# Kernel tuning notes

Measured on AMD Instinct MI355X. Metric: run time of the kernel, lower is better.

## Reference

```python
import jax, jax.numpy as jnp
import numpy as np

B, T, D, H, NL, V = 2, 2048, 512, 8, 4, 32000
HD = D // H
EPS = 1e-5


def _ln(x, g, b):
    mu = jnp.mean(x, axis=-1, keepdims=True)
    var = jnp.var(x, axis=-1, keepdims=True)
    return (x - mu) * jax.lax.rsqrt(var + EPS) * g + b


def setup_inputs() -> dict:
    key = jax.random.key(0)
    ks = jax.random.split(key, 16)
    f = lambda k, shp: jax.random.normal(k, shp, jnp.float32) * 0.02
    return {
        "token_ids": jax.random.randint(ks[0], (B, T), 0, V),
        "labels": jax.random.randint(ks[1], (B, T), 0, V),
        "tok_emb": f(ks[2], (V, D)),
        "pos_emb": f(ks[3], (T, D)),
        "Wq": f(ks[4], (NL, H, D, HD)),
        "Wk": f(ks[5], (NL, H, D, HD)),
        "Wv": f(ks[6], (NL, H, D, HD)),
        "Wo": f(ks[7], (NL, D, D)),
        "bo": jnp.zeros((NL, D), jnp.float32),
        "ln1_g": jnp.ones((NL, D), jnp.float32),
        "ln1_b": jnp.zeros((NL, D), jnp.float32),
        "ln2_g": jnp.ones((NL, D), jnp.float32),
        "ln2_b": jnp.zeros((NL, D), jnp.float32),
        "W1": f(ks[8], (NL, D, 4 * D)),
        "b1": jnp.zeros((NL, 4 * D), jnp.float32),
        "W2": f(ks[9], (NL, 4 * D, D)),
        "b2": jnp.zeros((NL, D), jnp.float32),
        "lnf_g": jnp.ones((D,), jnp.float32),
        "lnf_b": jnp.zeros((D,), jnp.float32),
        "Wp": f(ks[10], (D, V)),
        "bp": jnp.zeros((V,), jnp.float32),
    }


def reference(token_ids, labels, tok_emb, pos_emb, Wq, Wk, Wv, Wo, bo,
              ln1_g, ln1_b, ln2_g, ln2_b, W1, b1, W2, b2, lnf_g, lnf_b, Wp, bp):
    x = tok_emb[token_ids] + pos_emb[:T]            # (B, T, D)
    causal = jnp.tril(jnp.ones((T, T), bool))       # tril buffer
    scale = D ** -0.5                               # NOTE: source scales by dim_embed, not head_size
    for l in range(NL):
        xn = _ln(x, ln1_g[l], ln1_b[l])
        q = jnp.einsum('btd,hde->bhte', xn, Wq[l])  # (B, H, T, HD)
        k = jnp.einsum('btd,hde->bhte', xn, Wk[l])
        v = jnp.einsum('btd,hde->bhte', xn, Wv[l])
        w = jnp.einsum('bhte,bhse->bhts', q, k) * scale
        w = jnp.where(causal, w, -jnp.inf)
        w = jax.nn.softmax(w, axis=-1)
        o = jnp.einsum('bhts,bhse->bhte', w, v)     # (B, H, T, HD)
        o = o.transpose(0, 2, 1, 3).reshape(B, T, D)  # concat heads
        x = x + o @ Wo[l] + bo[l]
        xn = _ln(x, ln2_g[l], ln2_b[l])
        x = x + jax.nn.relu(xn @ W1[l] + b1[l]) @ W2[l] + b2[l]
    x = _ln(x, lnf_g, lnf_b)
    logits = x @ Wp + bp                            # (B, T, V)
    logits2d = logits.reshape(B * T, V)
    logp = jax.nn.log_softmax(logits2d, axis=-1)
    loss = -jnp.mean(logp[jnp.arange(B * T), labels.reshape(B * T)])
    return logits2d, loss
```

## Files before the change

### kernel.cpp

```cpp
#include <hip/hip_runtime.h>
#include <hip/hip_bf16.h>
#include <math.h>

#define B_ 2
#define T_ 2048
#define D_ 512
#define H_ 8
#define NL_ 4
#define V_ 32000
#define HD_ 64
#define BT_ (B_*T_)
#define EPS_ 1e-5f
#define SCALE_ 0.04419417382415922f
#define NEGBIG -1e30f

typedef __bf16 bf16x8 __attribute__((ext_vector_type(8)));
typedef float  f32x4  __attribute__((ext_vector_type(4)));

__device__ __forceinline__ unsigned short f2bf(float f) {
  union { float f; unsigned u; } v; v.f = f;
  unsigned r = v.u + 0x7fff + ((v.u >> 16) & 1);
  return (unsigned short)(r >> 16);
}
__device__ __forceinline__ float bf2f(unsigned short h) {
  union { unsigned u; float f; } c; c.u = ((unsigned)h) << 16; return c.f;
}

__device__ __forceinline__ void gl_lds16(const void* g, void* l) {
  __builtin_amdgcn_global_load_lds(
      (const __attribute__((address_space(1))) void*)g,
      (__attribute__((address_space(3))) void*)l, 16, 0, 0);
}

#define WAITVM(n) asm volatile("s_waitcnt vmcnt(" #n ")" ::: "memory")
#define WAITLG0   asm volatile("s_waitcnt lgkmcnt(0)" ::: "memory")

__global__ __launch_bounds__(256) void embed_kernel(
    const int* __restrict__ ids, const float* __restrict__ tok,
    const float* __restrict__ pos, unsigned short* __restrict__ x)
{
  int i = blockIdx.x * 256 + threadIdx.x;
  int c8 = i & 63;
  int bt = i >> 6;
  int t  = bt & (T_ - 1);
  const float4* tr = reinterpret_cast<const float4*>(tok + (size_t)ids[bt] * D_ + c8*8);
  const float4* pr = reinterpret_cast<const float4*>(pos + (size_t)t * D_ + c8*8);
  float4 a0 = tr[0], a1 = tr[1], p0 = pr[0], p1 = pr[1];
  ushort4 o0, o1;
  o0.x = f2bf(a0.x + p0.x); o0.y = f2bf(a0.y + p0.y);
  o0.z = f2bf(a0.z + p0.z); o0.w = f2bf(a0.w + p0.w);
  o1.x = f2bf(a1.x + p1.x); o1.y = f2bf(a1.y + p1.y);
  o1.z = f2bf(a1.z + p1.z); o1.w = f2bf(a1.w + p1.w);
  unsigned short* orow = x + (size_t)bt * D_ + c8*8;
  *reinterpret_cast<ushort4*>(orow)     = o0;
  *reinterpret_cast<ushort4*>(orow + 4) = o1;
}

__global__ __launch_bounds__(256) void ln_kernel(
    const unsigned short* __restrict__ x, const float* __restrict__ g,
    const float* __restrict__ b, unsigned short* __restrict__ out)
{
  int row  = blockIdx.x * 4 + (threadIdx.x >> 6);
  int lane = threadIdx.x & 63;
  const unsigned short* xr = x + (size_t)row * D_;
  ushort4 u0 = *reinterpret_cast<const ushort4*>(xr + lane*4);
  ushort4 u1 = *reinterpret_cast<const ushort4*>(xr + 256 + lane*4);
  float v0x = bf2f(u0.x), v0y = bf2f(u0.y), v0z = bf2f(u0.z), v0w = bf2f(u0.w);
  float v1x = bf2f(u1.x), v1y = bf2f(u1.y), v1z = bf2f(u1.z), v1w = bf2f(u1.w);
  float s = v0x + v0y + v0z + v0w + v1x + v1y + v1z + v1w;
  float q = v0x*v0x + v0y*v0y + v0z*v0z + v0w*v0w
          + v1x*v1x + v1y*v1y + v1z*v1z + v1w*v1w;
  #pragma unroll
  for (int off = 1; off < 64; off <<= 1) {
    s += __shfl_xor(s, off);
    q += __shfl_xor(q, off);
  }
  float mean = s * (1.0f / D_);
  float var  = q * (1.0f / D_) - mean * mean;
  float rs   = rsqrtf(var + EPS_);
  const float4* g4 = reinterpret_cast<const float4*>(g);
  const float4* b4 = reinterpret_cast<const float4*>(b);
  float4 gv0 = g4[lane], gv1 = g4[lane + 64];
  float4 bv0 = b4[lane], bv1 = b4[lane + 64];
  ushort4 p0, p1;
  p0.x = f2bf((v0x - mean) * rs * gv0.x + bv0.x);
  p0.y = f2bf((v0y - mean) * rs * gv0.y + bv0.y);
  p0.z = f2bf((v0z - mean) * rs * gv0.z + bv0.z);
  p0.w = f2bf((v0w - mean) * rs * gv0.w + bv0.w);
  p1.x = f2bf((v1x - mean) * rs * gv1.x + bv1.x);
  p1.y = f2bf((v1y - mean) * rs * gv1.y + bv1.y);
  p1.z = f2bf((v1z - mean) * rs * gv1.z + bv1.z);
  p1.w = f2bf((v1w - mean) * rs * gv1.w + bv1.w);
  unsigned short* orow = out + (size_t)row * D_;
  *reinterpret_cast<ushort4*>(orow + lane * 4)       = p0;
  *reinterpret_cast<ushort4*>(orow + 256 + lane * 4) = p1;
}

__global__ __launch_bounds__(256) void transpose_cast(
    const float* __restrict__ src, unsigned short* __restrict__ dst,
    int C, int R, long sstride, long dstride)
{
  src += (size_t)blockIdx.z * sstride;
  dst += (size_t)blockIdx.z * dstride;
  __shared__ float t[32][33];
  int r0 = blockIdx.x * 32, c0 = blockIdx.y * 32;
  int tx = threadIdx.x & 31, ty = threadIdx.x >> 5;
  #pragma unroll
  for (int i = 0; i < 4; i++)
    t[ty + i*8][tx] = src[(size_t)(r0 + ty + i*8) * C + c0 + tx];
  __syncthreads();
  #pragma unroll
  for (int i = 0; i < 4; i++)
    dst[(size_t)(c0 + ty + i*8) * R + r0 + tx] = f2bf(t[tx][ty + i*8]);
}

__global__ __launch_bounds__(256) void qkvw_transpose(
    const float* __restrict__ Wq, const float* __restrict__ Wk,
    const float* __restrict__ Wv, unsigned short* __restrict__ dst)
{
  int z = blockIdx.z; int l = z / 24; int rem = z % 24; int mat = rem >> 3; int h = rem & 7;
  const float* W = (mat == 0 ? Wq : (mat == 1 ? Wk : Wv)) + ((size_t)(l * 8 + h)) * D_ * HD_;
  unsigned short* d = dst + ((size_t)l * 1536 + mat * 512 + h * 64) * D_;
  __shared__ float t[32][33];
  int d0 = blockIdx.x * 32, e0 = blockIdx.y * 32;
  int tx = threadIdx.x & 31, ty = threadIdx.x >> 5;
  #pragma unroll
  for (int i = 0; i < 4; i++)
    t[ty + i*8][tx] = W[(size_t)(d0 + ty + i*8) * HD_ + e0 + tx];
  __syncthreads();
  #pragma unroll
  for (int i = 0; i < 4; i++)
    d[(size_t)(e0 + ty + i*8) * D_ + d0 + tx] = f2bf(t[tx][ty + i*8]);
}

__global__ __launch_bounds__(512, 4) void gemm_logits(
    const unsigned short* __restrict__ A,
    const unsigned short* __restrict__ Bt,
    int K, const float* __restrict__ bias,
    float* __restrict__ outF, int ldc,
    float2* __restrict__ ms, int npan)
{
  __shared__ __align__(16) char smem[49152];
  unsigned short* Abase = (unsigned short*)smem;
  unsigned short* Bbase = (unsigned short*)(smem + 16384);
  float* E = (float*)smem;
  float2* msL = (float2*)smem;

  const int tid = threadIdx.x;
  const int lane = tid & 63;
  const int lr = lane & 15, g = lane >> 4;
  const int wv = tid >> 6, wm = wv >> 2, wn = wv & 3;

  const int gx = gridDim.x;
  int id = blockIdx.y * gx + blockIdx.x;
  const int nwg = gx * gridDim.y;
  if ((nwg & 7) == 0) { const int q = nwg >> 3; id = (id & 7) * q + (id >> 3); }
  const int bm = (id % gx) * 128, bn = (id / gx) * 256, bnp = id / gx;

  const int schk = (lane & 3) ^ ((lane >> 3) & 3);
  const unsigned short* Ab = A  + (size_t)(bm + wv*16 + (lane >> 2)) * K + schk * 8;
  const unsigned short* Bb = Bt + (size_t)(bn + wv*16 + (lane >> 2)) * K + schk * 8;

#define STAGEL(s, sl)                                                       \
  { const int kof_ = (s) * 32;                                              \
    gl_lds16(Ab + kof_,                 Abase + (sl)*4096 + wv*512);        \
    gl_lds16(Bb + kof_,                 Bbase + (sl)*8192 + wv*512);        \
    gl_lds16(Bb + (size_t)128*K + kof_, Bbase + (sl)*8192 + 4096 + wv*512); }

  f32x4 acc[4][4];
  #pragma unroll
  for (int m = 0; m < 4; m++)
    #pragma unroll
    for (int n = 0; n < 4; n++)
      acc[m][n] = (f32x4){0.f, 0.f, 0.f, 0.f};

  const int nt = K >> 5;
  STAGEL(0, 0);

  const int slotx = (g ^ ((lr >> 1) & 3)) << 3;

  for (int t = 0; t < nt; ++t) {
    __builtin_amdgcn_sched_barrier(0);
    if (t + 1 < nt) { STAGEL(t + 1, (t + 1) & 1); WAITVM(3); }
    else            { WAITVM(0); }
    __builtin_amdgcn_sched_barrier(0);
    __builtin_amdgcn_s_barrier();
    __builtin_amdgcn_sched_barrier(0);

    const unsigned short* Ac = Abase + (t & 1)*4096;
    const unsigned short* Bc = Bbase + (t & 1)*8192;
    bf16x8 af[4], bfr[4];
    #pragma unroll
    for (int m = 0; m < 4; m++)
      af[m] = *reinterpret_cast<const bf16x8*>(&Ac[(wm*64 + m*16 + lr) * 32 + slotx]);
    #pragma unroll
    for (int n = 0; n < 4; n++)
      bfr[n] = *reinterpret_cast<const bf16x8*>(&Bc[(wn*64 + n*16 + lr) * 32 + slotx]);
    __builtin_amdgcn_s_setprio(1);
    #pragma unroll
    for (int m = 0; m < 4; m++)
      #pragma unroll
      for (int n = 0; n < 4; n++)
        acc[m][n] = __builtin_amdgcn_mfma_f32_16x16x32_bf16(af[m], bfr[n], acc[m][n], 0, 0, 0);
    __builtin_amdgcn_s_setprio(0);
    __builtin_amdgcn_sched_barrier(0);
    __builtin_amdgcn_s_barrier();
  }
#undef STAGEL

  #pragma unroll
  for (int n = 0; n < 4; n++) {
    const float bv = bias ? bias[bn + wn*64 + n*16 + lr] : 0.f;
    #pragma unroll
    for (int m = 0; m < 4; m++)
      #pragma unroll
      for (int r = 0; r < 4; r++)
        acc[m][n][r] += bv;
  }

  if (ms) {
    #pragma unroll
    for (int m = 0; m < 4; m++) {
      float vmax[4] = {NEGBIG, NEGBIG, NEGBIG, NEGBIG};
      #pragma unroll
      for (int n = 0; n < 4; n++)
        #pragma unroll
        for (int r = 0; r < 4; r++)
          vmax[r] = fmaxf(vmax[r], acc[m][n][r]);
      #pragma unroll
      for (int r = 0; r < 4; r++) {
        #pragma unroll
        for (int off = 1; off < 16; off <<= 1)
          vmax[r] = fmaxf(vmax[r], __shfl_xor(vmax[r], off));
      }
      float vsum[4] = {0.f, 0.f, 0.f, 0.f};
      #pragma unroll
      for (int n = 0; n < 4; n++)
        #pragma unroll
        for (int r = 0; r < 4; r++)
          vsum[r] += __expf(acc[m][n][r] - vmax[r]);
      #pragma unroll
      for (int r = 0; r < 4; r++) {
        #pragma unroll
        for (int off = 1; off < 16; off <<= 1)
          vsum[r] += __shfl_xor(vsum[r], off);
      }
      if (lr == 0) {
        #pragma unroll
        for (int r = 0; r < 4; r++)
          msL[(wm*64 + m*16 + g*4 + r) * 4 + wn] = make_float2(vmax[r], vsum[r]);
      }
    }
    __syncthreads();
    if (tid < 128) {
      float M = NEGBIG, S = 0.f;
      #pragma unroll
      for (int w = 0; w < 4; w++) {
        float2 e = msL[tid * 4 + w];
        float Mn = fmaxf(M, e.x);
        S = S * __expf(M - Mn) + e.y * __expf(e.x - Mn);
        M = Mn;
      }
      ms[(size_t)(bm + tid) * npan + bnp] = make_float2(M, S);
    }
  }

  #pragma unroll
  for (int c = 0; c < 4; ++c) {
    __syncthreads();
    if (wm == (c >> 1)) {
      const int mb = (c & 1) * 2;
      #pragma unroll
      for (int mm = 0; mm < 2; mm++)
        #pragma unroll
        for (int n = 0; n < 4; n++)
          #pragma unroll
          for (int r = 0; r < 4; r++)
            E[(mm*16 + g*4 + r) * 260 + wn*64 + n*16 + lr] = acc[mb + mm][n][r];
    }
    __syncthreads();
    #pragma unroll
    for (int rep = 0; rep < 4; rep++) {
      const int row = rep*8 + wv;
      f32x4 v = *reinterpret_cast<const f32x4*>(&E[row*260 + lane*4]);
      __builtin_nontemporal_store(
          v, reinterpret_cast<f32x4*>(&outF[(size_t)(bm + c*32 + row) * ldc + bn + lane*4]));
    }
  }
}

template<int BM_T, int BN_T, int WM, int WN>
__global__ __launch_bounds__(256) void gemm_pipe(
    const unsigned short* __restrict__ A,
    const unsigned short* __restrict__ Bt,
    int K,
    const float* __restrict__ bias,
    const unsigned short* __restrict__ resid,
    float* __restrict__ outF,
    unsigned short* __restrict__ outH,
    int ldc, int relu)
{
  constexpr int BKp = 64;
  constexpr int ALOADS = BM_T / 32;
  constexpr int BLOADS = BN_T / 32;
  constexpr int LOADS  = ALOADS + BLOADS;
  constexpr int MR = BM_T / (16 * WM);
  constexpr int NR = BN_T / (16 * WN);
  __shared__ __align__(16) unsigned short As[2][BM_T * BKp];
  __shared__ __align__(16) unsigned short Bs[2][BN_T * BKp];

  const int tid = threadIdx.x;
  const int lane = tid & 63, wv = tid >> 6;
  const int lr = lane & 15, g = lane >> 4;

  const int gx = gridDim.x;
  int id = blockIdx.y * gx + blockIdx.x;
  const int nwg = gx * gridDim.y;
  if ((nwg & 7) == 0) {
    const int q = nwg >> 3;
    id = (id & 7) * q + (id >> 3);
  }
  const int bm = (id % gx) * BM_T, bn = (id / gx) * BN_T;

  const int m0w = (wv / WN) * (BM_T / WM);
  const int n0w = (wv % WN) * (BN_T / WN);

  const int srow = wv*8 + (lane >> 3);
  const int schk = (lane & 7) ^ (lane >> 3);
  const unsigned short* Ab = A  + (size_t)(bm + srow) * K + schk * 8;
  const unsigned short* Bb = Bt + (size_t)(bn + srow) * K + schk * 8;

#define STAGEP(s, sl)                                                           \
  { const int kof_ = (s) * BKp;                                                 \
    _Pragma("unroll")                                                           \
    for (int i_ = 0; i_ < ALOADS; ++i_)                                         \
      gl_lds16(Ab + (size_t)(i_*32)*K + kof_, As[sl] + i_*2048 + wv*512);       \
    _Pragma("unroll")                                                           \
    for (int i_ = 0; i_ < BLOADS; ++i_)                                         \
      gl_lds16(Bb + (size_t)(i_*32)*K + kof_, Bs[sl] + i_*2048 + wv*512); }

  f32x4 acc[MR][NR];
  #pragma unroll
  for (int m = 0; m < MR; m++)
    #pragma unroll
    for (int n = 0; n < NR; n++)
      acc[m][n] = (f32x4){0.f, 0.f, 0.f, 0.f};

  const int nt = K >> 6;
  STAGEP(0, 0);

  for (int t = 0; t < nt; ++t) {
    __builtin_amdgcn_sched_barrier(0);
    if (t + 1 < nt) {
      STAGEP(t + 1, (t + 1) & 1);
      if constexpr (LOADS == 4) WAITVM(4);
      else if constexpr (LOADS == 6) WAITVM(6);
      else WAITVM(8);
    } else {
      WAITVM(0);
    }
    __builtin_amdgcn_sched_barrier(0);
    __builtin_amdgcn_s_barrier();
    __builtin_amdgcn_sched_barrier(0);

    const unsigned short* Ac = As[t & 1];
    const unsigned short* Bc = Bs[t & 1];
    #pragma unroll
    for (int kk = 0; kk < 2; ++kk) {
      const int sl = ((kk*4 + g) ^ (lr & 7)) << 3;
      bf16x8 af[MR], bfr[NR];
      #pragma unroll
      for (int m = 0; m < MR; m++)
        af[m] = *reinterpret_cast<const bf16x8*>(&Ac[(m0w + m*16 + lr) * BKp + sl]);
      #pragma unroll
      for (int n = 0; n < NR; n++)
        bfr[n] = *reinterpret_cast<const bf16x8*>(&Bc[(n0w + n*16 + lr) * BKp + sl]);
      __builtin_amdgcn_s_setprio(1);
      #pragma unroll
      for (int m = 0; m < MR; m++)
        #pragma unroll
        for (int n = 0; n < NR; n++)
          acc[m][n] = __builtin_amdgcn_mfma_f32_16x16x32_bf16(af[m], bfr[n], acc[m][n], 0, 0, 0);
      __builtin_amdgcn_s_setprio(0);
    }
    __builtin_amdgcn_sched_barrier(0);
    __builtin_amdgcn_s_barrier();
  }
#undef STAGEP

  const int cr = g * 4;
  const int cc = lr;
  #pragma unroll
  for (int m = 0; m < MR; m++) {
    #pragma unroll
    for (int n = 0; n < NR; n++) {
      int row = bm + m0w + m*16 + cr;
      int col = bn + n0w + n*16 + cc;
      f32x4 a = acc[m][n];
      #pragma unroll
      for (int r = 0; r < 4; r++) {
        float v = a[r];
        if (bias)  v += bias[col];
        if (resid) v += bf2f(resid[(size_t)(row + r) * ldc + col]);
        if (relu)  v = fmaxf(v, 0.f);
        if (outF)  outF[(size_t)(row + r) * ldc + col] = v;
        if (outH)  outH[(size_t)(row + r) * ldc + col] = f2bf(v);
      }
    }
  }
}

__global__ __launch_bounds__(512) void attn_mfma(
    const unsigned short* __restrict__ qkv,
    unsigned short* __restrict__ o,
    unsigned short* __restrict__ Opart,
    float2* __restrict__ ml)
{
  __shared__ __align__(16) unsigned short Ks[2][64*64];
  __shared__ __align__(16) unsigned short Vt[2][64*64];
  __shared__ __align__(16) unsigned short Ps[8][16*64];

  static const unsigned char ord[24] = {7,22,23,20,21,6,18,19,16,17,5,14,15,12,13,4,10,11,8,9,3,2,1,0};
  const int slot = ord[blockIdx.x];
  const int bh = blockIdx.y, bb = bh >> 3, hh = bh & 7;
  int qb, it0, itn, half;
  if (slot < 8) { qb = slot; it0 = 0; itn = 2*qb + 2; half = -1; }
  else { const int p = slot - 8; qb = 8 + (p >> 1); half = p & 1;
         const int nh = qb + 1; it0 = half * nh; itn = nh; }

  const int tid = threadIdx.x, lane = tid & 63, wv = tid >> 6;
  const int lr = lane & 15, g = lane >> 4;

  const unsigned short* qp = qkv + ((size_t)(bb*T_ + qb*128))*1536 + hh*64;
  const unsigned short* kp = qkv + ((size_t)bb*T_)*1536 + 512  + hh*64;
  const unsigned short* vp = qkv + ((size_t)bb*T_)*1536 + 1024 + hh*64;

  bf16x8 qf[2];
  qf[0] = *reinterpret_cast<const bf16x8*>(qp + (size_t)(wv*16 + lr)*1536 + g*8);
  qf[1] = *reinterpret_cast<const bf16x8*>(qp + (size_t)(wv*16 + lr)*1536 + 32 + g*8);

  const int krow = wv*8 + (lane >> 3);
  const int khb  = (lane & 7) ^ (lane >> 3);

#define STAGE_K(s0_, buf_)                                           \
  gl_lds16(kp + (size_t)((s0_)*64 + krow)*1536 + khb*8,              \
           (void*)(Ks[buf_] + wv*512));

  uint4 uvr;
#define LOAD_V(s0_)                                                  \
  uvr = *reinterpret_cast<const uint4*>(                             \
      vp + (size_t)((s0_)*64 + lane)*1536 + wv*8);

  f32x4 ov[4];
  #pragma unroll
  for (int n = 0; n < 4; n++) ov[n] = (f32x4){0.f, 0.f, 0.f, 0.f};
  float mrow[4] = {NEGBIG, NEGBIG, NEGBIG, NEGBIG};
  float lrow[4] = {0.f, 0.f, 0.f, 0.f};

  STAGE_K(it0, 0);
  LOAD_V(it0);

  for (int ii = 0; ii < itn; ++ii) {
    const int s0 = it0 + ii;
    const int cur = ii & 1;
    WAITVM(0);
    __builtin_amdgcn_sched_barrier(0);
    {
      union { uint4 v; unsigned short e[8]; } uv; uv.v = uvr;
      #pragma unroll
      for (int j = 0; j < 8; j++)
        Vt[cur][(wv*8 + j)*64 + (((lane >> 3) ^ j) << 3) + (lane & 7)] = uv.e[j];
    }
    WAITLG0;
    __builtin_amdgcn_sched_barrier(0);
    __builtin_amdgcn_s_barrier();
    __builtin_amdgcn_sched_barrier(0);

    if (ii + 1 < itn) {
      STAGE_K(s0 + 1, cur ^ 1);
      LOAD_V(s0 + 1);
    }

    f32x4 sf[4];
    #pragma unroll
    for (int n = 0; n < 4; n++) sf[n] = (f32x4){0.f, 0.f, 0.f, 0.f};
    __builtin_amdgcn_s_setprio(1);
    #pragma unroll
    for (int kk = 0; kk < 2; kk++) {
      #pragma unroll
      for (int n = 0; n < 4; n++) {
        const bf16x8 kf = *reinterpret_cast<const bf16x8*>(
            &Ks[cur][(n*16 + lr)*64 + (((kk*4 + g) ^ (lr & 7)) << 3)]);
        sf[n] = __builtin_amdgcn_mfma_f32_16x16x32_bf16(qf[kk], kf, sf[n], 0, 0, 0);
      }
    }
    __builtin_amdgcn_s_setprio(0);

    float sv[4][4];
    #pragma unroll
    for (int n = 0; n < 4; n++)
      #pragma unroll
      for (int r = 0; r < 4; r++) {
        const int kvg = s0*64 + n*16 + lr;
        const int qg  = qb*128 + wv*16 + g*4 + r;
        sv[n][r] = (kvg > qg) ? NEGBIG : sf[n][r] * SCALE_;
      }

    float aa[4];
    #pragma unroll
    for (int r = 0; r < 4; r++) {
      float pm = fmaxf(fmaxf(sv[0][r], sv[1][r]), fmaxf(sv[2][r], sv[3][r]));
      pm = fmaxf(pm, __shfl_xor(pm, 1));
      pm = fmaxf(pm, __shfl_xor(pm, 2));
      pm = fmaxf(pm, __shfl_xor(pm, 4));
      pm = fmaxf(pm, __shfl_xor(pm, 8));
      float mn = fmaxf(mrow[r], pm);
      aa[r] = __expf(mrow[r] - mn);
      mrow[r] = mn;
    }
    float rs[4] = {0.f, 0.f, 0.f, 0.f};
    #pragma unroll
    for (int n = 0; n < 4; n++)
      #pragma unroll
      for (int r = 0; r < 4; r++) {
        float p = __expf(sv[n][r] - mrow[r]);
        rs[r] += p;
        Ps[wv][(g*4 + r)*64 + ((((n << 1) + (lr >> 3)) ^ ((g*4 + r) & 7)) << 3) + (lr & 7)] = f2bf(p);
      }
    #pragma unroll
    for (int r = 0; r < 4; r++) {
      float s = rs[r];
      s += __shfl_xor(s, 1); s += __shfl_xor(s, 2);
      s += __shfl_xor(s, 4); s += __shfl_xor(s, 8);
      lrow[r] = lrow[r]*aa[r] + s;
    }
    #pragma unroll
    for (int n = 0; n < 4; n++)
      #pragma unroll
      for (int r = 0; r < 4; r++)
        ov[n][r] *= aa[r];

    __builtin_amdgcn_s_setprio(1);
    #pragma unroll
    for (int kk = 0; kk < 2; kk++) {
      const bf16x8 pf = *reinterpret_cast<const bf16x8*>(
          &Ps[wv][lr*64 + (((kk*4 + g) ^ (lr & 7)) << 3)]);
      #pragma unroll
      for (int n = 0; n < 4; n++) {
        const bf16x8 vf = *reinterpret_cast<const bf16x8*>(
            &Vt[cur][(n*16 + lr)*64 + (((kk*4 + g) ^ (lr & 7)) << 3)]);
        ov[n] = __builtin_amdgcn_mfma_f32_16x16x32_bf16(pf, vf, ov[n], 0, 0, 0);
      }
    }
    __builtin_amdgcn_s_setprio(0);
    __builtin_amdgcn_sched_barrier(0);
    __builtin_amdgcn_s_barrier();
  }
#undef STAGE_K
#undef LOAD_V

  if (half < 0) {
    #pragma unroll
    for (int r = 0; r < 4; r++) {
      float inv = 1.0f / lrow[r];
      size_t row = (size_t)(bb*T_ + qb*128 + wv*16 + g*4 + r);
      #pragma unroll
      for (int n = 0; n < 4; n++)
        o[row*D_ + hh*64 + n*16 + lr] = f2bf(ov[n][r] * inv);
    }
  } else {
    const int blk = bh*8 + (qb - 8);
    unsigned short* Od = Opart + ((size_t)blk*2 + half)*128*64;
    #pragma unroll
    for (int r = 0; r < 4; r++) {
      const int rloc = wv*16 + g*4 + r;
      #pragma unroll
      for (int n = 0; n < 4; n++)
        Od[rloc*64 + n*16 + lr] = f2bf(ov[n][r]);
      if (lr == 0)
        ml[((size_t)blk*2 + half)*128 + rloc] = make_float2(mrow[r], lrow[r]);
    }
  }
}

__global__ __launch_bounds__(256) void attn_merge(
    const unsigned short* __restrict__ Opart, const float2* __restrict__ ml,
    unsigned short* __restrict__ o)
{
  const int blk = blockIdx.x;
  const int bh = blk >> 3, qb = (blk & 7) + 8;
  const int bb = bh >> 3, hh = bh & 7;
  const int tid = threadIdx.x;
  const int row = tid >> 1, ch = (tid & 1) * 32;
  const unsigned short* O0 = Opart + ((size_t)blk*2 + 0)*128*64;
  const unsigned short* O1 = Opart + ((size_t)blk*2 + 1)*128*64;
  const float2 a = ml[(size_t)blk*2*128 + row];
  const float2 b = ml[((size_t)blk*2 + 1)*128 + row];
  const float M  = fmaxf(a.x, b.x);
  const float e0 = __expf(a.x - M), e1 = __expf(b.x - M);
  const float inv = 1.0f / (a.y*e0 + b.y*e1);
  unsigned short* orow = o + ((size_t)(bb*T_ + qb*128 + row))*D_ + hh*64 + ch;
  #pragma unroll
  for (int c = 0; c < 32; c += 4) {
    ushort4 u0 = *reinterpret_cast<const ushort4*>(&O0[row*64 + ch + c]);
    ushort4 u1 = *reinterpret_cast<const ushort4*>(&O1[row*64 + ch + c]);
    ushort4 pk;
    pk.x = f2bf((bf2f(u0.x)*e0 + bf2f(u1.x)*e1) * inv);
    pk.y = f2bf((bf2f(u0.y)*e0 + bf2f(u1.y)*e1) * inv);
    pk.z = f2bf((bf2f(u0.z)*e0 + bf2f(u1.z)*e1) * inv);
    pk.w = f2bf((bf2f(u0.w)*e0 + bf2f(u1.w)*e1) * inv);
    *reinterpret_cast<ushort4*>(&orow[c]) = pk;
  }
}

__global__ __launch_bounds__(256) void loss_merge_kernel(
    const float2* __restrict__ ms, const float* __restrict__ logits,
    const int* __restrict__ labels, float* __restrict__ rowloss, int npan)
{
  const int tid = threadIdx.x, lane = tid & 63, wid = tid >> 6;
  const int row = blockIdx.x * 4 + wid;
  float M = NEGBIG, S = 0.f;
  const float2* p = ms + (size_t)row * npan;
  for (int i = lane; i < npan; i += 64) {
    float2 e = p[i];
    float Mn = fmaxf(M, e.x);
    S = S * __expf(M - Mn) + e.y * __expf(e.x - Mn);
    M = Mn;
  }
  #pragma unroll
  for (int off = 1; off < 64; off <<= 1) {
    float Mo = __shfl_xor(M, off), So = __shfl_xor(S, off);
    float Mn = fmaxf(M, Mo);
    S = S * __expf(M - Mn) + So * __expf(Mo - Mn);
    M = Mn;
  }
  if (lane == 0)
    rowloss[row] = logits[(size_t)row * V_ + labels[row]] - M - logf(S);
}

__global__ __launch_bounds__(256) void loss_final_kernel(
    const float* __restrict__ rowloss, float* __restrict__ out)
{
  __shared__ float red[4];
  const int tid = threadIdx.x, lane = tid & 63, wid = tid >> 6;
  float s = 0.f;
  for (int i = tid; i < BT_; i += 256) s += rowloss[i];
  #pragma unroll
  for (int off = 1; off < 64; off <<= 1) s += __shfl_xor(s, off);
  if (lane == 0) red[wid] = s;
  __syncthreads();
  if (tid == 0) out[0] = -(red[0] + red[1] + red[2] + red[3]) * (1.0f / BT_);
}

extern "C" void kernel_launch(void* const* d_in, const int* in_sizes, int n_in,
                              void* d_out, int out_size, void* d_ws, size_t ws_size,
                              hipStream_t stream)
{
  (void)in_sizes; (void)n_in; (void)out_size; (void)ws_size;
  const int*   ids    = (const int*)d_in[0];
  const int*   labels = (const int*)d_in[1];
  const float* tok    = (const float*)d_in[2];
  const float* pos    = (const float*)d_in[3];
  const float* Wq     = (const float*)d_in[4];
  const float* Wk     = (const float*)d_in[5];
  const float* Wv     = (const float*)d_in[6];
  const float* Wo     = (const float*)d_in[7];
  const float* bo     = (const float*)d_in[8];
  const float* ln1g   = (const float*)d_in[9];
  const float* ln1b   = (const float*)d_in[10];
  const float* ln2g   = (const float*)d_in[11];
  const float* ln2b   = (const float*)d_in[12];
  const float* W1     = (const float*)d_in[13];
  const float* b1     = (const float*)d_in[14];
  const float* W2     = (const float*)d_in[15];
  const float* b2     = (const float*)d_in[16];
  const float* lnfg   = (const float*)d_in[17];
  const float* lnfb   = (const float*)d_in[18];
  const float* Wp     = (const float*)d_in[19];
  const float* bp     = (const float*)d_in[20];

  float* out = (float*)d_out;
  char* base = (char*)d_ws;
  unsigned short* x       = (unsigned short*)(base + 0);
  unsigned short* xn      = (unsigned short*)(base + 8388608);
  float*          rowloss = (float*)(base + 12582912);
  unsigned short* WqkvT   = (unsigned short*)(base + 12599296);
  unsigned short* W1T     = (unsigned short*)(base + 18890752);
  unsigned short* W2T     = (unsigned short*)(base + 27279360);
  unsigned short* WoT     = (unsigned short*)(base + 35667968);
  unsigned short* qkvh    = (unsigned short*)(base + 37765120);
  unsigned short* ob      = (unsigned short*)(base + 50348032);
  unsigned short* h1      = (unsigned short*)(base + 54542336);
  unsigned short* Opart   = (unsigned short*)(base + 54542336);
  float2*         mlbuf   = (float2*)(base + 62930944);
  unsigned short* WpT     = (unsigned short*)(base + 37765120);
  float2*         msbuf   = (float2*)(base + 12599296);

  embed_kernel<<<BT_ * D_ / 8 / 256, 256, 0, stream>>>(ids, tok, pos, x);

  qkvw_transpose<<<dim3(16, 2, 96), 256, 0, stream>>>(Wq, Wk, Wv, WqkvT);
  transpose_cast<<<dim3(16, 64, 4), 256, 0, stream>>>(W1, W1T, 2048, 512, 1048576, 1048576);
  transpose_cast<<<dim3(64, 16, 4), 256, 0, stream>>>(W2, W2T, 512, 2048, 1048576, 1048576);
  transpose_cast<<<dim3(16, 16, 4), 256, 0, stream>>>(Wo, WoT, 512, 512, 262144, 262144);

  for (int l = 0; l < NL_; l++) {
    ln_kernel<<<BT_ / 4, 256, 0, stream>>>(x, ln1g + l * D_, ln1b + l * D_, xn);
    gemm_pipe<64,64,2,2><<<dim3(64, 24), 256, 0, stream>>>(
        xn, WqkvT + (size_t)l * 1536 * 512, 512, nullptr, nullptr, nullptr, qkvh, 1536, 0);
    attn_mfma<<<dim3(24, B_ * H_), 512, 0, stream>>>(qkvh, ob, Opart, mlbuf);
    attn_merge<<<128, 256, 0, stream>>>(Opart, mlbuf, ob);
    gemm_pipe<64,64,2,2><<<dim3(64, 8), 256, 0, stream>>>(
        ob, WoT + (size_t)l * 512 * 512, 512, bo + l * D_, x, nullptr, x, D_, 0);
    ln_kernel<<<BT_ / 4, 256, 0, stream>>>(x, ln2g + l * D_, ln2b + l * D_, xn);
    gemm_pipe<64,64,2,2><<<dim3(64, 32), 256, 0, stream>>>(
        xn, W1T + (size_t)l * 2048 * 512, 512, b1 + l * 4 * D_, nullptr, nullptr, h1, 4 * D_, 1);
    gemm_pipe<64,64,2,2><<<dim3(64, 8), 256, 0, stream>>>(
        h1, W2T + (size_t)l * 512 * 2048, 2048, b2 + l * D_, x, nullptr, x, D_, 0);
  }

  transpose_cast<<<dim3(16, 1000, 1), 256, 0, stream>>>(Wp, WpT, 32000, 512, 0, 0);
  ln_kernel<<<BT_ / 4, 256, 0, stream>>>(x, lnfg, lnfb, xn);
  gemm_logits<<<dim3(32, 125), 512, 0, stream>>>(
      xn, WpT, 512, bp, out, V_, msbuf, 125);

  loss_merge_kernel<<<BT_ / 4, 256, 0, stream>>>(msbuf, out, labels, rowloss, 125);
  loss_final_kernel<<<1, 256, 0, stream>>>(rowloss, out + (size_t)BT_ * V_);
}
```

Measured before the change: 874.5 us.

## Rebalance causal attention work with finer KV splits via lookup tables

Replaces the old scheme (query blocks 8-15 split into two KV halves) with table-driven scheduling. Query blocks 6-11 are split into two KV chunks and 12-15 into up to four, giving 34 blocks per head instead of 24, each with at most about 12 KV iterations. The merge kernel now combines a variable number of partials (2 or 4) per row and the partial buffer region is moved. This aims to shorten the critical path and improve load balance across CUs, at the cost of more partial writes and merge traffic.

```diff
diff --git a/kernel.cpp b/kernel.cpp
--- a/kernel.cpp
+++ b/kernel.cpp
@@ -420,13 +420,17 @@
   __shared__ __align__(16) unsigned short Vt[2][64*64];
   __shared__ __align__(16) unsigned short Ps[8][16*64];
 
-  static const unsigned char ord[24] = {7,22,23,20,21,6,18,19,16,17,5,14,15,12,13,4,10,11,8,9,3,2,1,0};
-  const int slot = ord[blockIdx.x];
+  static const unsigned char sqb[34]  = {5,11,11,10,10,4,9,9,8,8,3,7,7,14,14,15,15,15,15,6,6,12,12,13,13,13,13,14,14,2,12,12,1,0};
+  static const unsigned char sit0[34] = {0,0,12,0,11,0,0,10,0,9,0,0,8,0,8,0,8,16,24,0,7,0,7,0,7,14,21,16,23,0,14,20,0,0};
+  static const unsigned char sitn[34] = {12,12,12,11,11,10,10,10,9,9,8,8,8,8,8,8,8,8,8,7,7,7,7,7,7,7,7,7,7,6,6,6,4,2};
+  static const unsigned char sps[34]  = {255,10,11,8,9,255,6,7,4,5,255,2,3,20,21,24,25,26,27,0,1,12,13,16,17,18,19,22,23,255,14,15,255,255};
+
+  const int slot = blockIdx.x;
   const int bh = blockIdx.y, bb = bh >> 3, hh = bh & 7;
-  int qb, it0, itn, half;
-  if (slot < 8) { qb = slot; it0 = 0; itn = 2*qb + 2; half = -1; }
-  else { const int p = slot - 8; qb = 8 + (p >> 1); half = p & 1;
-         const int nh = qb + 1; it0 = half * nh; itn = nh; }
+  const int qb  = sqb[slot];
+  const int it0 = sit0[slot];
+  const int itn = sitn[slot];
+  const int ps  = sps[slot];
 
   const int tid = threadIdx.x, lane = tid & 63, wv = tid >> 6;
   const int lr = lane & 15, g = lane >> 4;
@@ -559,7 +563,7 @@
 #undef STAGE_K
 #undef LOAD_V
 
-  if (half < 0) {
+  if (ps == 255) {
     #pragma unroll
     for (int r = 0; r < 4; r++) {
       float inv = 1.0f / lrow[r];
@@ -569,8 +573,8 @@
         o[row*D_ + hh*64 + n*16 + lr] = f2bf(ov[n][r] * inv);
     }
   } else {
-    const int blk = bh*8 + (qb - 8);
-    unsigned short* Od = Opart + ((size_t)blk*2 + half)*128*64;
+    const size_t blk = (size_t)bh*28 + ps;
+    unsigned short* Od = Opart + blk*128*64;
     #pragma unroll
     for (int r = 0; r < 4; r++) {
       const int rloc = wv*16 + g*4 + r;
@@ -578,7 +582,7 @@
       for (int n = 0; n < 4; n++)
         Od[rloc*64 + n*16 + lr] = f2bf(ov[n][r]);
       if (lr == 0)
-        ml[((size_t)blk*2 + half)*128 + rloc] = make_float2(mrow[r], lrow[r]);
+        ml[blk*128 + rloc] = make_float2(mrow[r], lrow[r]);
     }
   }
 }
@@ -587,28 +591,39 @@
     const unsigned short* __restrict__ Opart, const float2* __restrict__ ml,
     unsigned short* __restrict__ o)
 {
-  const int blk = blockIdx.x;
-  const int bh = blk >> 3, qb = (blk & 7) + 8;
+  const int j  = blockIdx.x;
+  const int bh = blockIdx.y;
+  const int qb = 6 + j;
   const int bb = bh >> 3, hh = bh & 7;
+  const int ns  = (qb < 12) ? 2 : 4;
+  const int psb = (qb < 12) ? (2*j) : (12 + (qb - 12)*4);
   const int tid = threadIdx.x;
   const int row = tid >> 1, ch = (tid & 1) * 32;
-  const unsigned short* O0 = Opart + ((size_t)blk*2 + 0)*128*64;
-  const unsigned short* O1 = Opart + ((size_t)blk*2 + 1)*128*64;
-  const float2 a = ml[(size_t)blk*2*128 + row];
-  const float2 b = ml[((size_t)blk*2 + 1)*128 + row];
-  const float M  = fmaxf(a.x, b.x);
-  const float e0 = __expf(a.x - M), e1 = __expf(b.x - M);
-  const float inv = 1.0f / (a.y*e0 + b.y*e1);
+
+  float mv[4], lv[4];
+  float M = NEGBIG;
+  for (int p = 0; p < ns; ++p) {
+    float2 e = ml[((size_t)bh*28 + psb + p)*128 + row];
+    mv[p] = e.x; lv[p] = e.y;
+    M = fmaxf(M, e.x);
+  }
+  float S = 0.f, ef[4];
+  for (int p = 0; p < ns; ++p) { ef[p] = __expf(mv[p] - M); S += lv[p]*ef[p]; }
+  const float inv = 1.0f / S;
+
   unsigned short* orow = o + ((size_t)(bb*T_ + qb*128 + row))*D_ + hh*64 + ch;
   #pragma unroll
   for (int c = 0; c < 32; c += 4) {
-    ushort4 u0 = *reinterpret_cast<const ushort4*>(&O0[row*64 + ch + c]);
-    ushort4 u1 = *reinterpret_cast<const ushort4*>(&O1[row*64 + ch + c]);
+    float a0 = 0.f, a1 = 0.f, a2 = 0.f, a3 = 0.f;
+    for (int p = 0; p < ns; ++p) {
+      const unsigned short* Op = Opart + ((size_t)bh*28 + psb + p)*128*64;
+      ushort4 u = *reinterpret_cast<const ushort4*>(&Op[row*64 + ch + c]);
+      a0 += bf2f(u.x)*ef[p]; a1 += bf2f(u.y)*ef[p];
+      a2 += bf2f(u.z)*ef[p]; a3 += bf2f(u.w)*ef[p];
+    }
     ushort4 pk;
-    pk.x = f2bf((bf2f(u0.x)*e0 + bf2f(u1.x)*e1) * inv);
-    pk.y = f2bf((bf2f(u0.y)*e0 + bf2f(u1.y)*e1) * inv);
-    pk.z = f2bf((bf2f(u0.z)*e0 + bf2f(u1.z)*e1) * inv);
-    pk.w = f2bf((bf2f(u0.w)*e0 + bf2f(u1.w)*e1) * inv);
+    pk.x = f2bf(a0 * inv); pk.y = f2bf(a1 * inv);
+    pk.z = f2bf(a2 * inv); pk.w = f2bf(a3 * inv);
     *reinterpret_cast<ushort4*>(&orow[c]) = pk;
   }
 }
@@ -692,7 +707,7 @@
   unsigned short* ob      = (unsigned short*)(base + 50348032);
   unsigned short* h1      = (unsigned short*)(base + 54542336);
   unsigned short* Opart   = (unsigned short*)(base + 54542336);
-  float2*         mlbuf   = (float2*)(base + 62930944);
+  float2*         mlbuf   = (float2*)(base + 61882368);
   unsigned short* WpT     = (unsigned short*)(base + 37765120);
   float2*         msbuf   = (float2*)(base + 12599296);
 
@@ -707,8 +722,8 @@
     ln_kernel<<<BT_ / 4, 256, 0, stream>>>(x, ln1g + l * D_, ln1b + l * D_, xn);
     gemm_pipe<64,64,2,2><<<dim3(64, 24), 256, 0, stream>>>(
         xn, WqkvT + (size_t)l * 1536 * 512, 512, nullptr, nullptr, nullptr, qkvh, 1536, 0);
-    attn_mfma<<<dim3(24, B_ * H_), 512, 0, stream>>>(qkvh, ob, Opart, mlbuf);
-    attn_merge<<<128, 256, 0, stream>>>(Opart, mlbuf, ob);
+    attn_mfma<<<dim3(34, B_ * H_), 512, 0, stream>>>(qkvh, ob, Opart, mlbuf);
+    attn_merge<<<dim3(10, B_ * H_), 256, 0, stream>>>(Opart, mlbuf, ob);
     gemm_pipe<64,64,2,2><<<dim3(64, 8), 256, 0, stream>>>(
         ob, WoT + (size_t)l * 512 * 512, 512, bo + l * D_, x, nullptr, x, D_, 0);
     ln_kernel<<<BT_ / 4, 256, 0, stream>>>(x, ln2g + l * D_, ln2b + l * D_, xn);
```

After: 873.1 us. Within noise of the previous version (-0.2%).
